# Performance work log

Measured on AMD Instinct MI355X. Metric: run time of the kernel, lower is better.

## Reference

```python
import jax, jax.numpy as jnp
from jax import lax
import numpy as np

# Dcls2_1d config (matches init_kwargs)
K_H, K_W = 3, 3          # base kernel size
DIL = 4                  # max dilation along dim 0 (learnable spacings)
LIM = DIL // 2           # each tap may move +/- LIM rows
KH_EFF = K_H + 2 * LIM   # constructed kernel height (7)
PAD_H = 1 + LIM          # user padding 1 adjusted by dilation//2 (as in _adjust_padding)
PAD_W = 1


def build_kernel(weight, P1):
    """Construct dense conv kernel by bilinear scatter of weights at
    continuous learnable row offsets P1. weight,P1: (O, I, K_H, K_W).
    Returns (O, I, KH_EFF, K_W)."""
    kh = jnp.arange(K_H, dtype=weight.dtype)[None, None, :, None]
    pos = kh + LIM + jnp.clip(P1, -LIM, LIM)      # continuous row position in [0, KH_EFF-1]
    p0 = jnp.floor(pos)
    frac = pos - p0                                # interpolation residual (grad flows to P)
    p0i = p0.astype(jnp.int32)
    oh0 = jax.nn.one_hot(p0i, KH_EFF, dtype=weight.dtype)        # (O,I,Kh,Kw,KH_EFF)
    oh1 = jax.nn.one_hot(p0i + 1, KH_EFF, dtype=weight.dtype)    # OOB rows -> all-zero row
    return (jnp.einsum('oihw,oihwk->oikw', weight * (1.0 - frac), oh0)
            + jnp.einsum('oihw,oihwk->oikw', weight * frac, oh1))


def setup_inputs() -> dict:
    key = jax.random.key(0)
    k1, k2, k3, k4 = jax.random.split(key, 4)
    x = jax.random.normal(k1, (16, 128, 64, 64), jnp.float32)
    weight = jax.random.normal(k2, (256, 128, 3, 3), jnp.float32) * 0.03
    bias = jax.random.normal(k3, (256,), jnp.float32) * 0.01
    # learnable positions span the allowed +/- LIM range to exercise interpolation
    P = jax.random.uniform(k4, (1, 256, 128, 3, 3), jnp.float32, -2.0, 2.0)
    return {"x": x, "weight": weight, "bias": bias, "P": P}


def reference(x, weight, bias, P):
    K = build_kernel(weight, P[0])
    out = lax.conv_general_dilated(
        x, K,
        window_strides=(1, 1),
        padding=((PAD_H, PAD_H), (PAD_W, PAD_W)),
        dimension_numbers=('NCHW', 'OIHW', 'NCHW'),
        feature_group_count=1)
    return out + bias[None, :, None, None]
```

## Files before the change

### kernel.cpp

```cpp
#include <hip/hip_runtime.h>
#include <hip/hip_bf16.h>

#define NIMG 16
#define CIN 128
#define COUT 256
#define HH 64
#define WW 64
#define KHE 7
#define KW_ 3
#define HP (HH + 6)
#define WP (WW + 2)
#define KDIM (CIN * KHE * KW_)
#define NKT 42

typedef __attribute__((ext_vector_type(8))) short short8;
typedef __attribute__((ext_vector_type(4))) float f32x4;

#define AS1(p) ((const __attribute__((address_space(1))) void*)(p))
#define AS3(p) ((__attribute__((address_space(3))) void*)(p))

__global__ void __launch_bounds__(256) pad_convert(const float* __restrict__ x,
                                                   ushort* __restrict__ xp) {
  const int bid = blockIdx.x;
  const int n = bid / HP, hp = bid % HP;
  const int h = hp - 3;
  ushort* dst = xp + (size_t)(n * HP + hp) * (WP * CIN);
  const int tid = threadIdx.x;

  if (h < 0 || h >= HH) {
    uint4* p = (uint4*)dst;
    uint4 z; z.x = z.y = z.z = z.w = 0u;
    for (int idx = tid; idx < (WP * CIN * 2) / 16; idx += 256) p[idx] = z;
    return;
  }

  __shared__ ushort t[CIN][WW + 1];
  for (int it = 0; it < (CIN * WW) / 256; ++it) {
    int flat = it * 256 + tid;
    int i = flat >> 6, w = flat & 63;
    float v = x[(((size_t)n * CIN + i) * HH + h) * WW + w];
    __hip_bfloat16 b = __float2bfloat16(v);
    t[i][w] = *(ushort*)&b;
  }
  __syncthreads();
  for (int it = 0; it < (WP * CIN) / 256; ++it) {
    int flat = it * 256 + tid;
    int wp = flat >> 7, i = flat & 127;
    int w = wp - 1;
    ushort v = (w < 0 || w >= WW) ? (ushort)0 : t[i][w];
    dst[flat] = v;
  }
}

__global__ void __launch_bounds__(256) build_kb(const float* __restrict__ weight,
                                                const float* __restrict__ P,
                                                ushort* __restrict__ kb2) {
  int idx = blockIdx.x * 256 + threadIdx.x;
  if (idx >= COUT * KW_ * CIN) return;
  int i = idx & 127;
  int kw = (idx >> 7) % 3;
  int o = idx / (KW_ * CIN);
  int base = (o * CIN + i) * 9 + kw;

  float a[KHE] = {0.f, 0.f, 0.f, 0.f, 0.f, 0.f, 0.f};
#pragma unroll
  for (int kh = 0; kh < 3; ++kh) {
    float wv = weight[base + kh * 3];
    float p = P[base + kh * 3];
    p = fminf(2.f, fmaxf(-2.f, p));
    float pos = (float)(kh + 2) + p;
    float fl = floorf(pos);
    float fr = pos - fl;
    int r0 = (int)fl;
    float c0 = wv * (1.f - fr);
    float c1 = wv * fr;
#pragma unroll
    for (int r = 0; r < KHE; ++r) {
      a[r] += ((r0 == r) ? c0 : 0.f) + ((r0 + 1 == r) ? c1 : 0.f);
    }
  }
#pragma unroll
  for (int r = 0; r < KHE; ++r) {
    __hip_bfloat16 b = __float2bfloat16(a[r]);
    int kslice = (r * 3 + kw) * 4 + (i >> 5);
    kb2[(size_t)kslice * 8192 + o * 32 + (i & 31)] = *(ushort*)&b;
  }
}

__global__ void __launch_bounds__(512, 2) dcls_gemm(const ushort* __restrict__ xp,
                                                    const ushort* __restrict__ kb2,
                                                    const float* __restrict__ bias,
                                                    float* __restrict__ out) {
  __shared__ __align__(16) ushort As[4][256 * 64];

  const int tid = threadIdx.x;
  const int lane = tid & 63;
  const int wv = tid >> 6;
  const int wr = wv >> 2;
  const int wc = wv & 3;
  const int g = lane >> 4;
  const int lm = lane & 15;
  const int m0 = blockIdx.x << 8;

  const int srow = tid >> 3;
  const int swz = ((tid & 7) ^ (srow & 7)) * 8;

  const ushort* pA[4];
#pragma unroll
  for (int j = 0; j < 4; ++j) {
    int r = j * 64 + srow;
    int m = m0 + r;
    int ni = m >> 12, hh = (m >> 6) & 63, ww = m & 63;
    pA[j] = xp + (size_t)((ni * HP + hh) * WP + ww) * CIN + swz;
  }

  const ushort* kbB = kb2 + (size_t)wc * 2048 + lm * 32 + g * 8;

#define STAGEA(buf, kt) do { \
    int kh_ = (kt) / 6; int rem_ = (kt) - kh_ * 6; \
    int kw2_ = rem_ >> 1; int ic_ = rem_ & 1; \
    int offA_ = (kh_ * WP + kw2_) * CIN + ic_ * 64; \
    _Pragma("unroll") \
    for (int j_ = 0; j_ < 4; ++j_) \
      __builtin_amdgcn_global_load_lds(AS1(pA[j_] + offA_), AS3(&As[buf][(j_ * 64 + wv * 8) * 64]), 16, 0, 0); \
  } while (0)

#define LOADB(dst, kt) do { \
    _Pragma("unroll") \
    for (int n_ = 0; n_ < 4; ++n_) \
      _Pragma("unroll") \
      for (int kk_ = 0; kk_ < 2; ++kk_) \
        dst[n_][kk_] = *(const short8*)(kbB + (size_t)((kt) * 2 + kk_) * 8192 + n_ * 512); \
  } while (0)

  f32x4 acc[8][4] = {};
  const int swzR = (lm & 7) << 4;

  short8 bf0[4][2], bf1[4][2];

#define TILE_MFMA(buf, bf) do { \
    const char* Ab = (const char*)&As[buf][0]; \
    _Pragma("unroll") \
    for (int half_ = 0; half_ < 2; ++half_) { \
      short8 af[4][2]; \
      _Pragma("unroll") \
      for (int m4_ = 0; m4_ < 4; ++m4_) \
        _Pragma("unroll") \
        for (int kk_ = 0; kk_ < 2; ++kk_) { \
          int rowA_ = wr * 128 + half_ * 64 + m4_ * 16 + lm; \
          af[m4_][kk_] = *(const short8*)(Ab + rowA_ * 128 + ((kk_ * 64 + g * 16) ^ swzR)); \
        } \
      _Pragma("unroll") \
      for (int kk_ = 0; kk_ < 2; ++kk_) \
        _Pragma("unroll") \
        for (int m4_ = 0; m4_ < 4; ++m4_) \
          _Pragma("unroll") \
          for (int n_ = 0; n_ < 4; ++n_) \
            acc[half_ * 4 + m4_][n_] = __builtin_amdgcn_mfma_f32_16x16x32_bf16( \
                af[m4_][kk_], bf[n_][kk_], acc[half_ * 4 + m4_][n_], 0, 0, 0); \
    } \
  } while (0)

#define SUBITER(kt, bfc) do { \
    __builtin_amdgcn_sched_barrier(0); \
    asm volatile("s_waitcnt vmcnt(12)" ::: "memory"); \
    __builtin_amdgcn_s_barrier(); \
    __builtin_amdgcn_sched_barrier(0); \
    { int ktn_ = ((kt) + 2 < NKT) ? (kt) + 2 : 0; \
      STAGEA(((kt) + 2) & 3, ktn_); \
      TILE_MFMA((kt) & 3, bfc); \
      LOADB(bfc, ktn_); } \
  } while (0)

  STAGEA(0, 0);
  LOADB(bf0, 0);
  STAGEA(1, 1);
  LOADB(bf1, 1);

  for (int kt = 0; kt < NKT; kt += 2) {
    SUBITER(kt, bf0);
    SUBITER(kt + 1, bf1);
  }
#undef SUBITER
#undef TILE_MFMA
#undef LOADB
#undef STAGEA

#pragma unroll
  for (int n_ = 0; n_ < 4; ++n_)
#pragma unroll
    for (int kk_ = 0; kk_ < 2; ++kk_) {
      asm volatile("" :: "v"((int)bf0[n_][kk_][0]));
      asm volatile("" :: "v"((int)bf1[n_][kk_][0]));
    }

#pragma unroll
  for (int fn = 0; fn < 4; ++fn) {
    int o = wc * 64 + fn * 16 + lm;
    float bv = bias[o];
#pragma unroll
    for (int fm = 0; fm < 8; ++fm) {
      int m = m0 + wr * 128 + fm * 16 + g * 4;
      int ni = m >> 12, hh = (m >> 6) & 63, ww = m & 63;
      f32x4 v = acc[fm][fn];
      v[0] += bv; v[1] += bv; v[2] += bv; v[3] += bv;
      *(f32x4*)(out + (size_t)((ni * COUT + o) * HH + hh) * WW + ww) = v;
    }
  }
}

extern "C" void kernel_launch(void* const* d_in, const int* in_sizes, int n_in,
                              void* d_out, int out_size, void* d_ws, size_t ws_size,
                              hipStream_t stream) {
  const float* x = (const float*)d_in[0];
  const float* weight = (const float*)d_in[1];
  const float* bias = (const float*)d_in[2];
  const float* P = (const float*)d_in[3];
  float* out = (float*)d_out;

  const size_t xp_elems = (size_t)NIMG * HP * WP * CIN;
  ushort* xp = (ushort*)d_ws;
  ushort* kb2 = (ushort*)((char*)d_ws + xp_elems * 2);

  hipLaunchKernelGGL(pad_convert, dim3(NIMG * HP), dim3(256), 0, stream, x, xp);
  hipLaunchKernelGGL(build_kb, dim3((COUT * KW_ * CIN + 255) / 256), dim3(256), 0, stream,
                     weight, P, kb2);
  hipLaunchKernelGGL(dcls_gemm, dim3(65536 / 256), dim3(512), 0, stream, xp, kb2, bias, out);
}
```

Before: 96.74 us.

## Shrink GEMM tile to 128x128 with triple-buffered LDS and swizzled block order

The convolution GEMM drops from a 256x256 output tile on 512 threads to a 128x128 tile on 256 threads. The grid grows to 1024 blocks, with block indices remapped so blocks sharing an output-channel half are grouped per XCD. LDS goes from four buffers to three, and the MFMA loop is split per k-half with an explicit lgkmcnt wait and s_setprio raised around the MFMA bursts. The aim is more resident blocks per CU for latency hiding and better load balance across CUs. The cost is less operand reuse per tile, so A and B are fetched more often, plus an extra barrier per k-step.

```diff
diff --git a/kernel.cpp b/kernel.cpp
--- a/kernel.cpp
+++ b/kernel.cpp
@@ -87,34 +87,38 @@
   }
 }
 
-__global__ void __launch_bounds__(512, 2) dcls_gemm(const ushort* __restrict__ xp,
+__global__ void __launch_bounds__(256, 3) dcls_gemm(const ushort* __restrict__ xp,
                                                     const ushort* __restrict__ kb2,
                                                     const float* __restrict__ bias,
                                                     float* __restrict__ out) {
-  __shared__ __align__(16) ushort As[4][256 * 64];
+  __shared__ __align__(16) ushort As[3][128 * 64];
 
   const int tid = threadIdx.x;
   const int lane = tid & 63;
   const int wv = tid >> 6;
-  const int wr = wv >> 2;
-  const int wc = wv & 3;
+  const int wr = wv >> 1;
+  const int wc = wv & 1;
   const int g = lane >> 4;
   const int lm = lane & 15;
-  const int m0 = blockIdx.x << 8;
-
-  const int srow = tid >> 3;
-  const int swz = ((tid & 7) ^ (srow & 7)) * 8;
+
+  const int bid = blockIdx.x;
+  const int lid = (bid & 7) * 128 + (bid >> 3);
+  const int mt = lid & 511;
+  const int nt = lid >> 9;
+  const int m0 = mt << 7;
+
+  const int swz = ((tid & 7) ^ ((tid >> 3) & 7)) * 8;
 
   const ushort* pA[4];
 #pragma unroll
   for (int j = 0; j < 4; ++j) {
-    int r = j * 64 + srow;
+    int r = j * 32 + (tid >> 3);
     int m = m0 + r;
     int ni = m >> 12, hh = (m >> 6) & 63, ww = m & 63;
     pA[j] = xp + (size_t)((ni * HP + hh) * WP + ww) * CIN + swz;
   }
 
-  const ushort* kbB = kb2 + (size_t)wc * 2048 + lm * 32 + g * 8;
+  const ushort* kbB = kb2 + (size_t)nt * 4096 + (size_t)wc * 2048 + lm * 32 + g * 8;
 
 #define STAGEA(buf, kt) do { \
     int kh_ = (kt) / 6; int rem_ = (kt) - kh_ * 6; \
@@ -122,7 +126,8 @@
     int offA_ = (kh_ * WP + kw2_) * CIN + ic_ * 64; \
     _Pragma("unroll") \
     for (int j_ = 0; j_ < 4; ++j_) \
-      __builtin_amdgcn_global_load_lds(AS1(pA[j_] + offA_), AS3(&As[buf][(j_ * 64 + wv * 8) * 64]), 16, 0, 0); \
+      __builtin_amdgcn_global_load_lds(AS1(pA[j_] + offA_), \
+          AS3(&As[buf][(j_ * 32 + wv * 8) * 64]), 16, 0, 0); \
   } while (0)
 
 #define LOADB(dst, kt) do { \
@@ -133,32 +138,29 @@
         dst[n_][kk_] = *(const short8*)(kbB + (size_t)((kt) * 2 + kk_) * 8192 + n_ * 512); \
   } while (0)
 
-  f32x4 acc[8][4] = {};
+  f32x4 acc[4][4] = {};
   const int swzR = (lm & 7) << 4;
 
   short8 bf0[4][2], bf1[4][2];
-
-#define TILE_MFMA(buf, bf) do { \
-    const char* Ab = (const char*)&As[buf][0]; \
-    _Pragma("unroll") \
-    for (int half_ = 0; half_ < 2; ++half_) { \
-      short8 af[4][2]; \
+  short8 af[4];
+
+#define HALF(Ab, bfc, kk) do { \
+    _Pragma("unroll") \
+    for (int m4_ = 0; m4_ < 4; ++m4_) { \
+      int rowA_ = wr * 64 + m4_ * 16 + lm; \
+      af[m4_] = *(const short8*)((Ab) + rowA_ * 128 + (((kk) * 64 + g * 16) ^ swzR)); \
+    } \
+    __builtin_amdgcn_sched_barrier(0); \
+    asm volatile("s_waitcnt lgkmcnt(0)" ::: "memory"); \
+    __builtin_amdgcn_sched_barrier(0); \
+    __builtin_amdgcn_s_setprio(1); \
+    _Pragma("unroll") \
+    for (int m4_ = 0; m4_ < 4; ++m4_) \
       _Pragma("unroll") \
-      for (int m4_ = 0; m4_ < 4; ++m4_) \
-        _Pragma("unroll") \
-        for (int kk_ = 0; kk_ < 2; ++kk_) { \
-          int rowA_ = wr * 128 + half_ * 64 + m4_ * 16 + lm; \
-          af[m4_][kk_] = *(const short8*)(Ab + rowA_ * 128 + ((kk_ * 64 + g * 16) ^ swzR)); \
-        } \
-      _Pragma("unroll") \
-      for (int kk_ = 0; kk_ < 2; ++kk_) \
-        _Pragma("unroll") \
-        for (int m4_ = 0; m4_ < 4; ++m4_) \
-          _Pragma("unroll") \
-          for (int n_ = 0; n_ < 4; ++n_) \
-            acc[half_ * 4 + m4_][n_] = __builtin_amdgcn_mfma_f32_16x16x32_bf16( \
-                af[m4_][kk_], bf[n_][kk_], acc[half_ * 4 + m4_][n_], 0, 0, 0); \
-    } \
+      for (int n_ = 0; n_ < 4; ++n_) \
+        acc[m4_][n_] = __builtin_amdgcn_mfma_f32_16x16x32_bf16( \
+            af[m4_], bfc[n_][kk], acc[m4_][n_], 0, 0, 0); \
+    __builtin_amdgcn_s_setprio(0); \
   } while (0)
 
 #define SUBITER(kt, bfc) do { \
@@ -166,10 +168,15 @@
     asm volatile("s_waitcnt vmcnt(12)" ::: "memory"); \
     __builtin_amdgcn_s_barrier(); \
     __builtin_amdgcn_sched_barrier(0); \
-    { int ktn_ = ((kt) + 2 < NKT) ? (kt) + 2 : 0; \
-      STAGEA(((kt) + 2) & 3, ktn_); \
-      TILE_MFMA((kt) & 3, bfc); \
-      LOADB(bfc, ktn_); } \
+    const char* Ab = (const char*)&As[(kt) % 3][0]; \
+    HALF(Ab, bfc, 0); \
+    HALF(Ab, bfc, 1); \
+    __builtin_amdgcn_sched_barrier(0); \
+    __builtin_amdgcn_s_barrier(); \
+    __builtin_amdgcn_sched_barrier(0); \
+    int ktn_ = ((kt) + 2 < NKT) ? (kt) + 2 : 0; \
+    STAGEA(((kt) + 2) % 3, ktn_); \
+    LOADB(bfc, ktn_); \
   } while (0)
 
   STAGEA(0, 0);
@@ -182,7 +189,7 @@
     SUBITER(kt + 1, bf1);
   }
 #undef SUBITER
-#undef TILE_MFMA
+#undef HALF
 #undef LOADB
 #undef STAGEA
 
@@ -196,11 +203,11 @@
 
 #pragma unroll
   for (int fn = 0; fn < 4; ++fn) {
-    int o = wc * 64 + fn * 16 + lm;
+    int o = nt * 128 + wc * 64 + fn * 16 + lm;
     float bv = bias[o];
 #pragma unroll
-    for (int fm = 0; fm < 8; ++fm) {
-      int m = m0 + wr * 128 + fm * 16 + g * 4;
+    for (int fm = 0; fm < 4; ++fm) {
+      int m = m0 + wr * 64 + fm * 16 + g * 4;
       int ni = m >> 12, hh = (m >> 6) & 63, ww = m & 63;
       f32x4 v = acc[fm][fn];
       v[0] += bv; v[1] += bv; v[2] += bv; v[3] += bv;
@@ -225,5 +232,5 @@
   hipLaunchKernelGGL(pad_convert, dim3(NIMG * HP), dim3(256), 0, stream, x, xp);
   hipLaunchKernelGGL(build_kb, dim3((COUT * KW_ * CIN + 255) / 256), dim3(256), 0, stream,
                      weight, P, kb2);
-  hipLaunchKernelGGL(dcls_gemm, dim3(65536 / 256), dim3(512), 0, stream, xp, kb2, bias, out);
-}
+  hipLaunchKernelGGL(dcls_gemm, dim3(1024), dim3(256), 0, stream, xp, kb2, bias, out);
+}
```

Result: slower. 221.2 us (+128.6%).
